# Kernel tuning notes

Hardware: AMD Instinct MI355X
Metric: run time of the kernel (lower is better)

The kernel has to match this reference:

```python
import jax, jax.numpy as jnp
import numpy as np

D_MODEL = 512
H = 8
D_K = D_MODEL // H


def setup_inputs() -> dict:
    key = jax.random.key(0)
    ks = jax.random.split(key, 11)
    B, S = 2, 4096
    scale = 1.0 / np.sqrt(D_MODEL)
    inp = {
        "q": jax.random.normal(ks[0], (B, S, D_MODEL), jnp.float32),
        "k": jax.random.normal(ks[1], (B, S, D_MODEL), jnp.float32),
        "v": jax.random.normal(ks[2], (B, S, D_MODEL), jnp.float32),
        "wq": jax.random.normal(ks[3], (D_MODEL, D_MODEL), jnp.float32) * scale,
        "bq": jnp.zeros((D_MODEL,), jnp.float32),
        "wk": jax.random.normal(ks[4], (D_MODEL, D_MODEL), jnp.float32) * scale,
        "bk": jnp.zeros((D_MODEL,), jnp.float32),
        "wv": jax.random.normal(ks[5], (D_MODEL, D_MODEL), jnp.float32) * scale,
        "bv": jnp.zeros((D_MODEL,), jnp.float32),
        "wo": jax.random.normal(ks[6], (D_MODEL, D_MODEL), jnp.float32) * scale,
        "bo": jnp.zeros((D_MODEL,), jnp.float32),
    }
    return inp


def reference(q, k, v, wq, bq, wk, bk, wv, bv, wo, bo):
    B, S, _ = q.shape
    # Linear projections (torch Linear: x @ W.T + b), split into heads -> [B,H,S,Dk]
    def proj(x, w, b):
        y = jnp.einsum('bsd,ed->bse', x, w) + b
        return y.reshape(B, -1, H, D_K).transpose(0, 2, 1, 3)

    qh = proj(q, wq, bq)
    kh = proj(k, wk, bk)
    vh = proj(v, wv, bv)

    # scaled dot-product attention, full [B,H,S,S] scores (faithful to source)
    scores = jnp.einsum('bhqd,bhkd->bhqk', qh, kh) / jnp.sqrt(jnp.asarray(D_K, qh.dtype))
    attn = jax.nn.softmax(scores, axis=-1)
    x = jnp.einsum('bhqk,bhkd->bhqd', attn, vh)

    # merge heads and output projection
    x = x.transpose(0, 2, 1, 3).reshape(B, S, H * D_K)
    return jnp.einsum('bsd,ed->bse', x, wo) + bo
```

## Files before the change

kernel.cpp:

```cpp
#include <hip/hip_runtime.h>

#define DM 512
#define NH 8
#define DK 64
#define SEQ 4096

typedef short bf16x8 __attribute__((ext_vector_type(8)));
typedef float f32x4 __attribute__((ext_vector_type(4)));
typedef unsigned short u16;
typedef u16 u16x8 __attribute__((ext_vector_type(8)));
typedef u16 u16x4 __attribute__((ext_vector_type(4)));
typedef unsigned int u32;
typedef u32 u32x2 __attribute__((ext_vector_type(2)));

__device__ __forceinline__ u16 f2bf(float f) {
  union { float f; unsigned u; } v; v.f = f;
  unsigned r = v.u + 0x7fffu + ((v.u >> 16) & 1u);
  return (u16)(r >> 16);
}

__device__ __forceinline__ u32 cvtpk(float a, float b) {
  u32 r; asm("v_cvt_pk_bf16_f32 %0, %1, %2" : "=v"(r) : "v"(a), "v"(b)); return r;
}

__device__ __forceinline__ float fexp2(float x) {
  float r; asm("v_exp_f32 %0, %1" : "=v"(r) : "v"(x)); return r;
}

__device__ __forceinline__ float fmax3(float a, float b, float c) {
  return fmaxf(fmaxf(a, b), c);
}

template<int MODE>
__global__ __launch_bounds__(256, 2)
void gemm_proj(const void* __restrict__ Xv, const float* __restrict__ W,
               const float* __restrict__ bias, void* __restrict__ Outv)
{
  __shared__ alignas(16) u16 Alds[64][72];
  __shared__ alignas(16) u16 Blds[128][72];
  const int t = threadIdx.x;
  const int bx = blockIdx.x & 127;
  const int by = blockIdx.x >> 7;
  const int m0 = bx << 6, n0 = by << 7;
  const int lane = t & 63, w = t >> 6;
  const int lr = lane & 15, lg = lane >> 4;
  const int wr = w >> 1, wc = w & 1;

  f32x4 acc[2][4];
  #pragma unroll
  for (int i = 0; i < 2; ++i)
    #pragma unroll
    for (int j = 0; j < 4; ++j) acc[i][j] = (f32x4){0.f, 0.f, 0.f, 0.f};

  float4 xa[4]; u16x8 xa3[2]; float4 wb[8];

  auto loadX = [&](int k0) {
    if (MODE < 3) {
      const float* X = (const float*)Xv;
      #pragma unroll
      for (int i = 0; i < 4; ++i) {
        int f = (i << 8) + t;
        xa[i] = *(const float4*)(X + (size_t)(m0 + (f >> 4)) * 512 + k0 + ((f & 15) << 2));
      }
    } else {
      const u16* X = (const u16*)Xv;
      #pragma unroll
      for (int i = 0; i < 2; ++i) {
        int f = (i << 8) + t;
        xa3[i] = *(const u16x8*)(X + (size_t)(m0 + (f >> 3)) * 512 + k0 + ((f & 7) << 3));
      }
    }
    #pragma unroll
    for (int i = 0; i < 8; ++i) {
      int f = (i << 8) + t;
      wb[i] = *(const float4*)(W + (size_t)(n0 + (f >> 4)) * 512 + k0 + ((f & 15) << 2));
    }
  };

  loadX(0);
  for (int k0 = 0; k0 < 512; k0 += 64) {
    __syncthreads();
    if (MODE < 3) {
      #pragma unroll
      for (int i = 0; i < 4; ++i) {
        int f = (i << 8) + t;
        u16x4 p = { f2bf(xa[i].x), f2bf(xa[i].y), f2bf(xa[i].z), f2bf(xa[i].w) };
        *(u16x4*)&Alds[f >> 4][(f & 15) << 2] = p;
      }
    } else {
      #pragma unroll
      for (int i = 0; i < 2; ++i) {
        int f = (i << 8) + t;
        *(u16x8*)&Alds[f >> 3][(f & 7) << 3] = xa3[i];
      }
    }
    #pragma unroll
    for (int i = 0; i < 8; ++i) {
      int f = (i << 8) + t;
      u16x4 p = { f2bf(wb[i].x), f2bf(wb[i].y), f2bf(wb[i].z), f2bf(wb[i].w) };
      *(u16x4*)&Blds[f >> 4][(f & 15) << 2] = p;
    }
    __syncthreads();
    if (k0 + 64 < 512) loadX(k0 + 64);

    #pragma unroll
    for (int kk = 0; kk < 2; ++kk) {
      bf16x8 af[2], bfr[4];
      #pragma unroll
      for (int mi = 0; mi < 2; ++mi)
        af[mi] = *(const bf16x8*)&Alds[(wr << 5) + (mi << 4) + lr][(kk << 5) + (lg << 3)];
      #pragma unroll
      for (int ni = 0; ni < 4; ++ni)
        bfr[ni] = *(const bf16x8*)&Blds[(wc << 6) + (ni << 4) + lr][(kk << 5) + (lg << 3)];
      #pragma unroll
      for (int mi = 0; mi < 2; ++mi)
        #pragma unroll
        for (int ni = 0; ni < 4; ++ni)
          acc[mi][ni] = __builtin_amdgcn_mfma_f32_16x16x32_bf16(af[mi], bfr[ni], acc[mi][ni], 0, 0, 0);
    }
  }

  #pragma unroll
  for (int mi = 0; mi < 2; ++mi) {
    #pragma unroll
    for (int ni = 0; ni < 4; ++ni) {
      const int e = n0 + (wc << 6) + (ni << 4) + lr;
      const int m = m0 + (wr << 5) + (mi << 4) + (lg << 2);
      const float bb = bias[e];
      if (MODE == 0 || MODE == 1) {
        u16* O = (u16*)Outv;
        const int b = m >> 12, s = m & 4095, h = e >> 6, dk = e & 63;
        size_t base = ((size_t)((b << 3) + h) * SEQ + s) * DK + dk;
        #pragma unroll
        for (int r = 0; r < 4; ++r) {
          float val = acc[mi][ni][r] + bb;
          if (MODE == 0) val *= 0.18033688f;
          O[base + (size_t)r * DK] = f2bf(val);
        }
      } else if (MODE == 2) {
        u16* O = (u16*)Outv;
        const int b = m >> 12, s = m & 4095, h = e >> 6, dk = e & 63;
        size_t base = ((size_t)((b << 3) + h) * DK + dk) * SEQ + s;
        u16x4 p = { f2bf(acc[mi][ni][0] + bb), f2bf(acc[mi][ni][1] + bb),
                    f2bf(acc[mi][ni][2] + bb), f2bf(acc[mi][ni][3] + bb) };
        *(u16x4*)(O + base) = p;
      } else {
        float* O = (float*)Outv;
        size_t base = (size_t)m * 512 + e;
        #pragma unroll
        for (int r = 0; r < 4; ++r) O[base + (size_t)r * 512] = acc[mi][ni][r] + bb;
      }
    }
  }
}

__global__ __launch_bounds__(256, 2)
void attn_kernel(const u16* __restrict__ Qh, const u16* __restrict__ Kh,
                 const u16* __restrict__ Vt, u16* __restrict__ Xa)
{
  __shared__ alignas(16) u16 smem[12800];

  const int t = threadIdx.x;
  const int lane = t & 63, w = t >> 6;
  const int lr = lane & 15, lg = lane >> 4;
  const int ob = ((blockIdx.x & 7) << 6) + (blockIdx.x >> 3);
  const int qb = ob & 31, bh = ob >> 5;
  const size_t qkbase = (size_t)bh * SEQ * DK;
  const size_t vbase  = (size_t)bh * DK * SEQ;
  u16* Pw = smem + 8192 + w * 1152;

  bf16x8 qf[2][2];
  #pragma unroll
  for (int mi = 0; mi < 2; ++mi)
    #pragma unroll
    for (int kk = 0; kk < 2; ++kk) {
      int qrow = (qb << 7) + (w << 5) + (mi << 4) + lr;
      qf[mi][kk] = *(const bf16x8*)(Qh + qkbase + (size_t)qrow * DK + (kk << 5) + (lg << 3));
    }

  bf16x8 onesf;
  {
    u16 one = (lr == 0) ? (u16)0x3F80 : (u16)0;
    #pragma unroll
    for (int j = 0; j < 8; ++j) onesf[j] = (short)one;
  }

  float mrun[2] = {-3e38f, -3e38f};
  f32x4 o[2][4], osum[2];
  #pragma unroll
  for (int mi = 0; mi < 2; ++mi) {
    #pragma unroll
    for (int dt = 0; dt < 4; ++dt) o[mi][dt] = (f32x4){0.f, 0.f, 0.f, 0.f};
    osum[mi] = (f32x4){0.f, 0.f, 0.f, 0.f};
  }

  const u16* Kg = Kh + qkbase;
  const u16* Vg = Vt + vbase;
  const int r0 = t >> 3, c0 = t & 7;
  const int r1 = r0 + 32, c1 = c0;
  const int wk0 = r0 * 64 + ((c0 ^ (r0 & 7)) << 3);
  const int wk1 = r1 * 64 + ((c1 ^ (r1 & 7)) << 3);

  u16x8 kr0, kr1, vr0, vr1;
  kr0 = *(const u16x8*)(Kg + (size_t)r0 * 64 + (c0 << 3));
  kr1 = *(const u16x8*)(Kg + (size_t)r1 * 64 + (c1 << 3));
  vr0 = *(const u16x8*)(Vg + (size_t)r0 * SEQ + (c0 << 3));
  vr1 = *(const u16x8*)(Vg + (size_t)r1 * SEQ + (c1 << 3));

  for (int it = 0; it < SEQ / 64; ++it) {
    __syncthreads();
    *(u16x8*)&smem[wk0]        = kr0;
    *(u16x8*)&smem[wk1]        = kr1;
    *(u16x8*)&smem[4096 + wk0] = vr0;
    *(u16x8*)&smem[4096 + wk1] = vr1;
    __syncthreads();
    if (it + 1 < SEQ / 64) {
      const int kv0n = (it + 1) << 6;
      kr0 = *(const u16x8*)(Kg + (size_t)(kv0n + r0) * 64 + (c0 << 3));
      kr1 = *(const u16x8*)(Kg + (size_t)(kv0n + r1) * 64 + (c1 << 3));
      vr0 = *(const u16x8*)(Vg + (size_t)r0 * SEQ + kv0n + (c0 << 3));
      vr1 = *(const u16x8*)(Vg + (size_t)r1 * SEQ + kv0n + (c1 << 3));
    }

    bf16x8 kf[4][2], vf[4][2];
    #pragma unroll
    for (int nt = 0; nt < 4; ++nt)
      #pragma unroll
      for (int kk = 0; kk < 2; ++kk) {
        const int off = ((nt << 4) + lr) * 64 + ((((kk << 2) + lg) ^ (lr & 7)) << 3);
        kf[nt][kk] = *(const bf16x8*)&smem[off];
        vf[nt][kk] = *(const bf16x8*)&smem[4096 + off];
      }

    #pragma unroll
    for (int mi = 0; mi < 2; ++mi) {
      f32x4 s[4];
      #pragma unroll
      for (int nt = 0; nt < 4; ++nt) s[nt] = (f32x4){0.f, 0.f, 0.f, 0.f};
      #pragma unroll
      for (int kk = 0; kk < 2; ++kk)
        #pragma unroll
        for (int nt = 0; nt < 4; ++nt)
          s[nt] = __builtin_amdgcn_mfma_f32_16x16x32_bf16(kf[nt][kk], qf[mi][kk], s[nt], 0, 0, 0);

      float m0 = fmax3(s[0][0], s[0][1], s[0][2]);
      float m1 = fmax3(s[0][3], s[1][0], s[1][1]);
      float m2 = fmax3(s[1][2], s[1][3], s[2][0]);
      float m3 = fmax3(s[2][1], s[2][2], s[2][3]);
      float m4 = fmax3(s[3][0], s[3][1], s[3][2]);
      float tmax = fmaxf(fmax3(m0, m1, m2), fmax3(m3, m4, s[3][3]));
      tmax = fmaxf(tmax, __shfl_xor(tmax, 16));
      tmax = fmaxf(tmax, __shfl_xor(tmax, 32));

      if (!__all(tmax <= mrun[mi] + 8.f)) {
        float mnew = fmaxf(mrun[mi], tmax);
        float scl = fexp2(mrun[mi] - mnew);
        mrun[mi] = mnew;
        osum[mi][0] *= scl;
        #pragma unroll
        for (int dt = 0; dt < 4; ++dt) o[mi][dt] *= scl;
      }
      const float mm = mrun[mi];

      #pragma unroll
      for (int nt = 0; nt < 4; ++nt) {
        float e0 = fexp2(s[nt][0] - mm), e1 = fexp2(s[nt][1] - mm);
        float e2 = fexp2(s[nt][2] - mm), e3 = fexp2(s[nt][3] - mm);
        u32x2 pk2 = { cvtpk(e0, e1), cvtpk(e2, e3) };
        *(u32x2*)((char*)Pw + lr * 144 + (nt << 5) + (lg << 3)) = pk2;
      }

      #pragma unroll
      for (int kk = 0; kk < 2; ++kk) {
        bf16x8 pf = *(const bf16x8*)&Pw[lr * 72 + (kk << 5) + (lg << 3)];
        #pragma unroll
        for (int dt = 0; dt < 4; ++dt)
          o[mi][dt] = __builtin_amdgcn_mfma_f32_16x16x32_bf16(vf[dt][kk], pf, o[mi][dt], 0, 0, 0);
        osum[mi] = __builtin_amdgcn_mfma_f32_16x16x32_bf16(onesf, pf, osum[mi], 0, 0, 0);
      }
    }
  }
  __syncthreads();

  #pragma unroll
  for (int mi = 0; mi < 2; ++mi) {
    float lsum = __shfl(osum[mi][0], lr);
    float inv = 1.f / lsum;
    #pragma unroll
    for (int dt = 0; dt < 4; ++dt) {
      u16x4 v4 = { f2bf(o[mi][dt][0] * inv), f2bf(o[mi][dt][1] * inv),
                   f2bf(o[mi][dt][2] * inv), f2bf(o[mi][dt][3] * inv) };
      int row = (w << 5) + (mi << 4) + lr;
      *(u16x4*)&smem[row * 72 + (dt << 4) + (lg << 2)] = v4;
    }
  }
  __syncthreads();
  {
    const int b = bh >> 3, h = bh & 7;
    #pragma unroll
    for (int i = 0; i < 4; ++i) {
      int f = (i << 8) + t;
      int row = f >> 3, c8 = (f & 7) << 3;
      u16x8 val = *(const u16x8*)&smem[row * 72 + c8];
      *(u16x8*)(Xa + ((size_t)b * SEQ + (qb << 7) + row) * DM + (h << 6) + c8) = val;
    }
  }
}

extern "C" void kernel_launch(void* const* d_in, const int* in_sizes, int n_in,
                              void* d_out, int out_size, void* d_ws, size_t ws_size,
                              hipStream_t stream)
{
  const float* q  = (const float*)d_in[0];
  const float* k  = (const float*)d_in[1];
  const float* v  = (const float*)d_in[2];
  const float* wq = (const float*)d_in[3];
  const float* bq = (const float*)d_in[4];
  const float* wk = (const float*)d_in[5];
  const float* bk = (const float*)d_in[6];
  const float* wv = (const float*)d_in[7];
  const float* bv = (const float*)d_in[8];
  const float* wo = (const float*)d_in[9];
  const float* bo = (const float*)d_in[10];

  const size_t HS = (size_t)2 * NH * SEQ * DK;
  u16* Qh = (u16*)d_ws;
  u16* Kh = Qh + HS;
  u16* Vt = Kh + HS;
  u16* Xa = Vt + HS;

  gemm_proj<0><<<512, 256, 0, stream>>>(q, wq, bq, Qh);
  gemm_proj<1><<<512, 256, 0, stream>>>(k, wk, bk, Kh);
  gemm_proj<2><<<512, 256, 0, stream>>>(v, wv, bv, Vt);
  attn_kernel<<<512, 256, 0, stream>>>(Qh, Kh, Vt, Xa);
  gemm_proj<3><<<512, 256, 0, stream>>>(Xa, wo, bo, (float*)d_out);
}
```

Measured before the change: 155.7 us.

## Merge QKV projections into one launch and widen attention KV tile to 128

The three Q/K/V projection GEMMs become a single 1536-block launch that picks inputs and output layout by block index. This removes two launches and lets the three projections fill the GPU together. The attention kernel now stages 128 keys per iteration instead of 64, with a wider swizzled V tile and separate P buffers for the two query sub-tiles. It also raises wave priority around the MFMA blocks. This halves the number of barriers and softmax max-reductions per key, at the cost of more LDS (about 66 KB), which may reduce occupancy, and more registers for score accumulators.

```diff
diff --git a/kernel.cpp b/kernel.cpp
--- a/kernel.cpp
+++ b/kernel.cpp
@@ -31,16 +31,117 @@
   return fmaxf(fmaxf(a, b), c);
 }
 
-template<int MODE>
 __global__ __launch_bounds__(256, 2)
-void gemm_proj(const void* __restrict__ Xv, const float* __restrict__ W,
-               const float* __restrict__ bias, void* __restrict__ Outv)
+void gemm_qkv(const float* __restrict__ qx, const float* __restrict__ kx,
+              const float* __restrict__ vx,
+              const float* __restrict__ wq, const float* __restrict__ bq,
+              const float* __restrict__ wk, const float* __restrict__ bk,
+              const float* __restrict__ wv, const float* __restrict__ bv,
+              u16* __restrict__ Qh, u16* __restrict__ Kh, u16* __restrict__ Vt)
+{
+  __shared__ alignas(16) u16 Alds[64][72];
+  __shared__ alignas(16) u16 Blds[128][72];
+  const int mode = blockIdx.x >> 9;
+  const int bid = blockIdx.x & 511;
+  const float* X = (mode == 0) ? qx : (mode == 1) ? kx : vx;
+  const float* W = (mode == 0) ? wq : (mode == 1) ? wk : wv;
+  const float* Bs = (mode == 0) ? bq : (mode == 1) ? bk : bv;
+
+  const int t = threadIdx.x;
+  const int bx = bid & 127, by = bid >> 7;
+  const int m0 = bx << 6, n0 = by << 7;
+  const int lane = t & 63, w = t >> 6;
+  const int lr = lane & 15, lg = lane >> 4;
+  const int wr = w >> 1, wc = w & 1;
+
+  f32x4 acc[2][4];
+  #pragma unroll
+  for (int i = 0; i < 2; ++i)
+    #pragma unroll
+    for (int j = 0; j < 4; ++j) acc[i][j] = (f32x4){0.f, 0.f, 0.f, 0.f};
+
+  float4 xa[4]; float4 wb[8];
+  auto loadX = [&](int k0) {
+    #pragma unroll
+    for (int i = 0; i < 4; ++i) {
+      int f = (i << 8) + t;
+      xa[i] = *(const float4*)(X + (size_t)(m0 + (f >> 4)) * 512 + k0 + ((f & 15) << 2));
+    }
+    #pragma unroll
+    for (int i = 0; i < 8; ++i) {
+      int f = (i << 8) + t;
+      wb[i] = *(const float4*)(W + (size_t)(n0 + (f >> 4)) * 512 + k0 + ((f & 15) << 2));
+    }
+  };
+
+  loadX(0);
+  for (int k0 = 0; k0 < 512; k0 += 64) {
+    __syncthreads();
+    #pragma unroll
+    for (int i = 0; i < 4; ++i) {
+      int f = (i << 8) + t;
+      u16x4 p = { f2bf(xa[i].x), f2bf(xa[i].y), f2bf(xa[i].z), f2bf(xa[i].w) };
+      *(u16x4*)&Alds[f >> 4][(f & 15) << 2] = p;
+    }
+    #pragma unroll
+    for (int i = 0; i < 8; ++i) {
+      int f = (i << 8) + t;
+      u16x4 p = { f2bf(wb[i].x), f2bf(wb[i].y), f2bf(wb[i].z), f2bf(wb[i].w) };
+      *(u16x4*)&Blds[f >> 4][(f & 15) << 2] = p;
+    }
+    __syncthreads();
+    if (k0 + 64 < 512) loadX(k0 + 64);
+
+    #pragma unroll
+    for (int kk = 0; kk < 2; ++kk) {
+      bf16x8 af[2], bfr[4];
+      #pragma unroll
+      for (int mi = 0; mi < 2; ++mi)
+        af[mi] = *(const bf16x8*)&Alds[(wr << 5) + (mi << 4) + lr][(kk << 5) + (lg << 3)];
+      #pragma unroll
+      for (int ni = 0; ni < 4; ++ni)
+        bfr[ni] = *(const bf16x8*)&Blds[(wc << 6) + (ni << 4) + lr][(kk << 5) + (lg << 3)];
+      #pragma unroll
+      for (int mi = 0; mi < 2; ++mi)
+        #pragma unroll
+        for (int ni = 0; ni < 4; ++ni)
+          acc[mi][ni] = __builtin_amdgcn_mfma_f32_16x16x32_bf16(af[mi], bfr[ni], acc[mi][ni], 0, 0, 0);
+    }
+  }
+
+  const float sc = (mode == 0) ? 0.18033688f : 1.0f;
+  #pragma unroll
+  for (int mi = 0; mi < 2; ++mi) {
+    #pragma unroll
+    for (int ni = 0; ni < 4; ++ni) {
+      const int e = n0 + (wc << 6) + (ni << 4) + lr;
+      const int m = m0 + (wr << 5) + (mi << 4) + (lg << 2);
+      const float bb = Bs[e];
+      const int b = m >> 12, s = m & 4095, h = e >> 6, dk = e & 63;
+      if (mode != 2) {
+        u16* O = (mode == 0) ? Qh : Kh;
+        size_t base = ((size_t)((b << 3) + h) * SEQ + s) * DK + dk;
+        #pragma unroll
+        for (int r = 0; r < 4; ++r)
+          O[base + (size_t)r * DK] = f2bf((acc[mi][ni][r] + bb) * sc);
+      } else {
+        size_t base = ((size_t)((b << 3) + h) * DK + dk) * SEQ + s;
+        u16x4 p = { f2bf(acc[mi][ni][0] + bb), f2bf(acc[mi][ni][1] + bb),
+                    f2bf(acc[mi][ni][2] + bb), f2bf(acc[mi][ni][3] + bb) };
+        *(u16x4*)(Vt + base) = p;
+      }
+    }
+  }
+}
+
+__global__ __launch_bounds__(256, 2)
+void gemm_out(const u16* __restrict__ Xa, const float* __restrict__ W,
+              const float* __restrict__ bias, float* __restrict__ Out)
 {
   __shared__ alignas(16) u16 Alds[64][72];
   __shared__ alignas(16) u16 Blds[128][72];
   const int t = threadIdx.x;
-  const int bx = blockIdx.x & 127;
-  const int by = blockIdx.x >> 7;
+  const int bx = blockIdx.x & 127, by = blockIdx.x >> 7;
   const int m0 = bx << 6, n0 = by << 7;
   const int lane = t & 63, w = t >> 6;
   const int lr = lane & 15, lg = lane >> 4;
@@ -52,23 +153,12 @@
     #pragma unroll
     for (int j = 0; j < 4; ++j) acc[i][j] = (f32x4){0.f, 0.f, 0.f, 0.f};
 
-  float4 xa[4]; u16x8 xa3[2]; float4 wb[8];
-
+  u16x8 xa3[2]; float4 wb[8];
   auto loadX = [&](int k0) {
-    if (MODE < 3) {
-      const float* X = (const float*)Xv;
-      #pragma unroll
-      for (int i = 0; i < 4; ++i) {
-        int f = (i << 8) + t;
-        xa[i] = *(const float4*)(X + (size_t)(m0 + (f >> 4)) * 512 + k0 + ((f & 15) << 2));
-      }
-    } else {
-      const u16* X = (const u16*)Xv;
-      #pragma unroll
-      for (int i = 0; i < 2; ++i) {
-        int f = (i << 8) + t;
-        xa3[i] = *(const u16x8*)(X + (size_t)(m0 + (f >> 3)) * 512 + k0 + ((f & 7) << 3));
-      }
+    #pragma unroll
+    for (int i = 0; i < 2; ++i) {
+      int f = (i << 8) + t;
+      xa3[i] = *(const u16x8*)(Xa + (size_t)(m0 + (f >> 3)) * 512 + k0 + ((f & 7) << 3));
     }
     #pragma unroll
     for (int i = 0; i < 8; ++i) {
@@ -80,19 +170,10 @@
   loadX(0);
   for (int k0 = 0; k0 < 512; k0 += 64) {
     __syncthreads();
-    if (MODE < 3) {
-      #pragma unroll
-      for (int i = 0; i < 4; ++i) {
-        int f = (i << 8) + t;
-        u16x4 p = { f2bf(xa[i].x), f2bf(xa[i].y), f2bf(xa[i].z), f2bf(xa[i].w) };
-        *(u16x4*)&Alds[f >> 4][(f & 15) << 2] = p;
-      }
-    } else {
-      #pragma unroll
-      for (int i = 0; i < 2; ++i) {
-        int f = (i << 8) + t;
-        *(u16x8*)&Alds[f >> 3][(f & 7) << 3] = xa3[i];
-      }
+    #pragma unroll
+    for (int i = 0; i < 2; ++i) {
+      int f = (i << 8) + t;
+      *(u16x8*)&Alds[f >> 3][(f & 7) << 3] = xa3[i];
     }
     #pragma unroll
     for (int i = 0; i < 8; ++i) {
@@ -127,29 +208,9 @@
       const int e = n0 + (wc << 6) + (ni << 4) + lr;
       const int m = m0 + (wr << 5) + (mi << 4) + (lg << 2);
       const float bb = bias[e];
-      if (MODE == 0 || MODE == 1) {
-        u16* O = (u16*)Outv;
-        const int b = m >> 12, s = m & 4095, h = e >> 6, dk = e & 63;
-        size_t base = ((size_t)((b << 3) + h) * SEQ + s) * DK + dk;
-        #pragma unroll
-        for (int r = 0; r < 4; ++r) {
-          float val = acc[mi][ni][r] + bb;
-          if (MODE == 0) val *= 0.18033688f;
-          O[base + (size_t)r * DK] = f2bf(val);
-        }
-      } else if (MODE == 2) {
-        u16* O = (u16*)Outv;
-        const int b = m >> 12, s = m & 4095, h = e >> 6, dk = e & 63;
-        size_t base = ((size_t)((b << 3) + h) * DK + dk) * SEQ + s;
-        u16x4 p = { f2bf(acc[mi][ni][0] + bb), f2bf(acc[mi][ni][1] + bb),
-                    f2bf(acc[mi][ni][2] + bb), f2bf(acc[mi][ni][3] + bb) };
-        *(u16x4*)(O + base) = p;
-      } else {
-        float* O = (float*)Outv;
-        size_t base = (size_t)m * 512 + e;
-        #pragma unroll
-        for (int r = 0; r < 4; ++r) O[base + (size_t)r * 512] = acc[mi][ni][r] + bb;
-      }
+      size_t base = (size_t)m * 512 + e;
+      #pragma unroll
+      for (int r = 0; r < 4; ++r) Out[base + (size_t)r * 512] = acc[mi][ni][r] + bb;
     }
   }
 }
@@ -158,7 +219,7 @@
 void attn_kernel(const u16* __restrict__ Qh, const u16* __restrict__ Kh,
                  const u16* __restrict__ Vt, u16* __restrict__ Xa)
 {
-  __shared__ alignas(16) u16 smem[12800];
+  __shared__ alignas(16) u16 smem[33792];
 
   const int t = threadIdx.x;
   const int lane = t & 63, w = t >> 6;
@@ -167,7 +228,8 @@
   const int qb = ob & 31, bh = ob >> 5;
   const size_t qkbase = (size_t)bh * SEQ * DK;
   const size_t vbase  = (size_t)bh * DK * SEQ;
-  u16* Pw = smem + 8192 + w * 1152;
+  u16* P0 = smem + 16384 + w * 4352;
+  u16* P1 = P0 + 2176;
 
   bf16x8 qf[2][2];
   #pragma unroll
@@ -196,88 +258,110 @@
 
   const u16* Kg = Kh + qkbase;
   const u16* Vg = Vt + vbase;
-  const int r0 = t >> 3, c0 = t & 7;
-  const int r1 = r0 + 32, c1 = c0;
-  const int wk0 = r0 * 64 + ((c0 ^ (r0 & 7)) << 3);
-  const int wk1 = r1 * 64 + ((c1 ^ (r1 & 7)) << 3);
-
-  u16x8 kr0, kr1, vr0, vr1;
-  kr0 = *(const u16x8*)(Kg + (size_t)r0 * 64 + (c0 << 3));
-  kr1 = *(const u16x8*)(Kg + (size_t)r1 * 64 + (c1 << 3));
-  vr0 = *(const u16x8*)(Vg + (size_t)r0 * SEQ + (c0 << 3));
-  vr1 = *(const u16x8*)(Vg + (size_t)r1 * SEQ + (c1 << 3));
-
-  for (int it = 0; it < SEQ / 64; ++it) {
-    __syncthreads();
-    *(u16x8*)&smem[wk0]        = kr0;
-    *(u16x8*)&smem[wk1]        = kr1;
-    *(u16x8*)&smem[4096 + wk0] = vr0;
-    *(u16x8*)&smem[4096 + wk1] = vr1;
-    __syncthreads();
-    if (it + 1 < SEQ / 64) {
-      const int kv0n = (it + 1) << 6;
-      kr0 = *(const u16x8*)(Kg + (size_t)(kv0n + r0) * 64 + (c0 << 3));
-      kr1 = *(const u16x8*)(Kg + (size_t)(kv0n + r1) * 64 + (c1 << 3));
-      vr0 = *(const u16x8*)(Vg + (size_t)r0 * SEQ + kv0n + (c0 << 3));
-      vr1 = *(const u16x8*)(Vg + (size_t)r1 * SEQ + kv0n + (c1 << 3));
-    }
-
-    bf16x8 kf[4][2], vf[4][2];
-    #pragma unroll
-    for (int nt = 0; nt < 4; ++nt)
-      #pragma unroll
-      for (int kk = 0; kk < 2; ++kk) {
-        const int off = ((nt << 4) + lr) * 64 + ((((kk << 2) + lg) ^ (lr & 7)) << 3);
-        kf[nt][kk] = *(const bf16x8*)&smem[off];
-        vf[nt][kk] = *(const bf16x8*)&smem[4096 + off];
+  int kro[4], kco[4], kdst[4], vro[4], vco[4], vdst[4];
+  #pragma unroll
+  for (int i = 0; i < 4; ++i) {
+    int G = t + (i << 8);
+    int kr = G >> 3, kc = G & 7;
+    int vr = G >> 4, vc = G & 15;
+    kro[i] = kr; kco[i] = kc << 3;
+    vro[i] = vr; vco[i] = vc << 3;
+    kdst[i] = kr * 64 + ((kc ^ (kr & 7)) << 3);
+    vdst[i] = 8192 + vr * 128 + ((vc ^ (vr & 15)) << 3);
+  }
+
+  u16x8 kpr[4], vpr[4];
+  #pragma unroll
+  for (int i = 0; i < 4; ++i) {
+    kpr[i] = *(const u16x8*)(Kg + (size_t)kro[i] * 64 + kco[i]);
+    vpr[i] = *(const u16x8*)(Vg + (size_t)vro[i] * SEQ + vco[i]);
+  }
+
+  auto softmax_store = [&](f32x4* s, float& mr, f32x4* oo, f32x4& os, u16* P) {
+    float tm[8];
+    #pragma unroll
+    for (int nt = 0; nt < 8; ++nt)
+      tm[nt] = fmaxf(fmax3(s[nt][0], s[nt][1], s[nt][2]), s[nt][3]);
+    float tmax = fmax3(fmax3(tm[0], tm[1], tm[2]), fmax3(tm[3], tm[4], tm[5]),
+                       fmaxf(tm[6], tm[7]));
+    tmax = fmaxf(tmax, __shfl_xor(tmax, 16));
+    tmax = fmaxf(tmax, __shfl_xor(tmax, 32));
+    if (!__all(tmax <= mr + 8.f)) {
+      float mnew = fmaxf(mr, tmax);
+      float scl = fexp2(mr - mnew);
+      mr = mnew;
+      os[0] *= scl;
+      #pragma unroll
+      for (int dt = 0; dt < 4; ++dt) oo[dt] *= scl;
+    }
+    const float mm = mr;
+    #pragma unroll
+    for (int nt = 0; nt < 8; ++nt) {
+      float e0 = fexp2(s[nt][0] - mm), e1 = fexp2(s[nt][1] - mm);
+      float e2 = fexp2(s[nt][2] - mm), e3 = fexp2(s[nt][3] - mm);
+      u32x2 pk2 = { cvtpk(e0, e1), cvtpk(e2, e3) };
+      *(u32x2*)((char*)P + lr * 272 + (nt << 5) + (lg << 3)) = pk2;
+    }
+  };
+
+  for (int it = 0; it < SEQ / 128; ++it) {
+    __syncthreads();
+    #pragma unroll
+    for (int i = 0; i < 4; ++i) {
+      *(u16x8*)&smem[kdst[i]] = kpr[i];
+      *(u16x8*)&smem[vdst[i]] = vpr[i];
+    }
+    __syncthreads();
+    if (it + 1 < SEQ / 128) {
+      const int kv0n = (it + 1) << 7;
+      #pragma unroll
+      for (int i = 0; i < 4; ++i) {
+        kpr[i] = *(const u16x8*)(Kg + (size_t)(kv0n + kro[i]) * 64 + kco[i]);
+        vpr[i] = *(const u16x8*)(Vg + (size_t)vro[i] * SEQ + kv0n + vco[i]);
       }
-
-    #pragma unroll
-    for (int mi = 0; mi < 2; ++mi) {
-      f32x4 s[4];
-      #pragma unroll
-      for (int nt = 0; nt < 4; ++nt) s[nt] = (f32x4){0.f, 0.f, 0.f, 0.f};
-      #pragma unroll
-      for (int kk = 0; kk < 2; ++kk)
-        #pragma unroll
-        for (int nt = 0; nt < 4; ++nt)
-          s[nt] = __builtin_amdgcn_mfma_f32_16x16x32_bf16(kf[nt][kk], qf[mi][kk], s[nt], 0, 0, 0);
-
-      float m0 = fmax3(s[0][0], s[0][1], s[0][2]);
-      float m1 = fmax3(s[0][3], s[1][0], s[1][1]);
-      float m2 = fmax3(s[1][2], s[1][3], s[2][0]);
-      float m3 = fmax3(s[2][1], s[2][2], s[2][3]);
-      float m4 = fmax3(s[3][0], s[3][1], s[3][2]);
-      float tmax = fmaxf(fmax3(m0, m1, m2), fmax3(m3, m4, s[3][3]));
-      tmax = fmaxf(tmax, __shfl_xor(tmax, 16));
-      tmax = fmaxf(tmax, __shfl_xor(tmax, 32));
-
-      if (!__all(tmax <= mrun[mi] + 8.f)) {
-        float mnew = fmaxf(mrun[mi], tmax);
-        float scl = fexp2(mrun[mi] - mnew);
-        mrun[mi] = mnew;
-        osum[mi][0] *= scl;
-        #pragma unroll
-        for (int dt = 0; dt < 4; ++dt) o[mi][dt] *= scl;
-      }
-      const float mm = mrun[mi];
-
-      #pragma unroll
-      for (int nt = 0; nt < 4; ++nt) {
-        float e0 = fexp2(s[nt][0] - mm), e1 = fexp2(s[nt][1] - mm);
-        float e2 = fexp2(s[nt][2] - mm), e3 = fexp2(s[nt][3] - mm);
-        u32x2 pk2 = { cvtpk(e0, e1), cvtpk(e2, e3) };
-        *(u32x2*)((char*)Pw + lr * 144 + (nt << 5) + (lg << 3)) = pk2;
-      }
-
-      #pragma unroll
-      for (int kk = 0; kk < 2; ++kk) {
-        bf16x8 pf = *(const bf16x8*)&Pw[lr * 72 + (kk << 5) + (lg << 3)];
-        #pragma unroll
-        for (int dt = 0; dt < 4; ++dt)
-          o[mi][dt] = __builtin_amdgcn_mfma_f32_16x16x32_bf16(vf[dt][kk], pf, o[mi][dt], 0, 0, 0);
-        osum[mi] = __builtin_amdgcn_mfma_f32_16x16x32_bf16(onesf, pf, osum[mi], 0, 0, 0);
-      }
+    }
+
+    f32x4 s0[8], s1[8];
+    #pragma unroll
+    for (int nt = 0; nt < 8; ++nt) {
+      s0[nt] = (f32x4){0.f, 0.f, 0.f, 0.f};
+      s1[nt] = (f32x4){0.f, 0.f, 0.f, 0.f};
+    }
+    #pragma unroll
+    for (int nt = 0; nt < 8; ++nt) {
+      const int row = ((nt << 4) + lr) * 64;
+      bf16x8 kf0 = *(const bf16x8*)&smem[row + ((lg ^ (lr & 7)) << 3)];
+      bf16x8 kf1 = *(const bf16x8*)&smem[row + (((4 + lg) ^ (lr & 7)) << 3)];
+      __builtin_amdgcn_s_setprio(1);
+      s0[nt] = __builtin_amdgcn_mfma_f32_16x16x32_bf16(kf0, qf[0][0], s0[nt], 0, 0, 0);
+      s0[nt] = __builtin_amdgcn_mfma_f32_16x16x32_bf16(kf1, qf[0][1], s0[nt], 0, 0, 0);
+      s1[nt] = __builtin_amdgcn_mfma_f32_16x16x32_bf16(kf0, qf[1][0], s1[nt], 0, 0, 0);
+      s1[nt] = __builtin_amdgcn_mfma_f32_16x16x32_bf16(kf1, qf[1][1], s1[nt], 0, 0, 0);
+      __builtin_amdgcn_s_setprio(0);
+    }
+
+    softmax_store(s0, mrun[0], o[0], osum[0], P0);
+    softmax_store(s1, mrun[1], o[1], osum[1], P1);
+
+    #pragma unroll
+    for (int kk = 0; kk < 4; ++kk) {
+      bf16x8 vf[4];
+      #pragma unroll
+      for (int dt = 0; dt < 4; ++dt)
+        vf[dt] = *(const bf16x8*)&smem[8192 + ((dt << 4) + lr) * 128 +
+                                       ((((kk << 2) + lg) ^ lr) << 3)];
+      bf16x8 pf0 = *(const bf16x8*)&P0[lr * 136 + (kk << 5) + (lg << 3)];
+      bf16x8 pf1 = *(const bf16x8*)&P1[lr * 136 + (kk << 5) + (lg << 3)];
+      __builtin_amdgcn_s_setprio(1);
+      #pragma unroll
+      for (int dt = 0; dt < 4; ++dt)
+        o[0][dt] = __builtin_amdgcn_mfma_f32_16x16x32_bf16(vf[dt], pf0, o[0][dt], 0, 0, 0);
+      osum[0] = __builtin_amdgcn_mfma_f32_16x16x32_bf16(onesf, pf0, osum[0], 0, 0, 0);
+      #pragma unroll
+      for (int dt = 0; dt < 4; ++dt)
+        o[1][dt] = __builtin_amdgcn_mfma_f32_16x16x32_bf16(vf[dt], pf1, o[1][dt], 0, 0, 0);
+      osum[1] = __builtin_amdgcn_mfma_f32_16x16x32_bf16(onesf, pf1, osum[1], 0, 0, 0);
+      __builtin_amdgcn_s_setprio(0);
     }
   }
   __syncthreads();
@@ -329,9 +413,7 @@
   u16* Vt = Kh + HS;
   u16* Xa = Vt + HS;
 
-  gemm_proj<0><<<512, 256, 0, stream>>>(q, wq, bq, Qh);
-  gemm_proj<1><<<512, 256, 0, stream>>>(k, wk, bk, Kh);
-  gemm_proj<2><<<512, 256, 0, stream>>>(v, wv, bv, Vt);
+  gemm_qkv<<<1536, 256, 0, stream>>>(q, k, v, wq, bq, wk, bk, wv, bv, Qh, Kh, Vt);
   attn_kernel<<<512, 256, 0, stream>>>(Qh, Kh, Vt, Xa);
-  gemm_proj<3><<<512, 256, 0, stream>>>(Xa, wo, bo, (float*)d_out);
-}
+  gemm_out<<<512, 256, 0, stream>>>(Xa, wo, bo, (float*)d_out);
+}
```

After: 150.0 us. -3.7%, faster.
